# Performance work log

Measured on AMD Instinct MI355X. Metric: run time of the kernel, lower is better.

The kernel has to match this reference:

```python
import jax, jax.numpy as jnp
import numpy as np
import math

HIDDEN = 2048
NUM_HEADS = 16
HEAD_SIZE = HIDDEN // NUM_HEADS
BATCH = 2
SEQ = 2048


def setup_inputs() -> dict:
    key = jax.random.key(0)
    k_x, k_wq, k_bq, k_wo, k_bo = jax.random.split(key, 5)
    scale_in = 1.0 / math.sqrt(HIDDEN)
    return {
        "x": jax.random.normal(k_x, (BATCH, SEQ, HIDDEN), dtype=jnp.float32),
        # torch Linear stored as W[out,in]; we keep the jax-friendly transpose [in,out]
        "Wqkv": jax.random.normal(k_wq, (HIDDEN, 3 * HIDDEN), dtype=jnp.float32) * scale_in,
        "bqkv": jax.random.normal(k_bq, (3 * HIDDEN,), dtype=jnp.float32) * 0.01,
        "Wo": jax.random.normal(k_wo, (HIDDEN, HIDDEN), dtype=jnp.float32) * scale_in,
        "bo": jax.random.normal(k_bo, (HIDDEN,), dtype=jnp.float32) * 0.01,
    }


def reference(x, Wqkv, bqkv, Wo, bo):
    b, s, _ = x.shape
    # fused QKV projection; channel layout is (three, num_heads, head_size)
    kqv = x @ Wqkv + bqkv                      # [b, s, 3*hidden]
    kqv = kqv.reshape(b, s, 3, NUM_HEADS, HEAD_SIZE)
    q = kqv[:, :, 0]                           # [b, s, n, h]
    k = kqv[:, :, 1]
    v = kqv[:, :, 2]
    # scores[b, n, s_key, t_query] = K_s . Q_t, scaled
    scores = jnp.einsum('bsnh,btnh->bnst', k, q) / math.sqrt(HEAD_SIZE)
    # faithful to original: keep upper triangle (key <= query), masked entries are exactly -10000
    ones = jnp.ones_like(scores)
    scores = jnp.triu(scores) + (-10000.0) * jnp.tril(ones, k=-1)
    attn = jax.nn.softmax(scores, axis=2)      # softmax over key dim
    out = jnp.einsum('bnkq,bknh->bqnh', attn, v)  # [b, s, n, h]
    out = out.reshape(b, s, NUM_HEADS * HEAD_SIZE)
    return out @ Wo + bo
```

## Files before the change

### kernel.cpp

```cpp
#include <hip/hip_runtime.h>
#include <hip/hip_bf16.h>

typedef __hip_bfloat16 bf16;
typedef __attribute__((ext_vector_type(8))) short short8;
typedef __attribute__((ext_vector_type(8))) unsigned short ushort8;
typedef __attribute__((ext_vector_type(4))) float floatx4;

#define BATCH 2
#define S_LEN 2048
#define NHEAD 16
#define HD 128
#define HIDDEN 2048
#define QSCALE 0.12754435f

static __device__ __forceinline__ unsigned short f2bf(float f) {
    union { float f; unsigned int u; } c; c.f = f;
    unsigned int u = c.u;
    unsigned int rounded = u + 0x7FFF + ((u >> 16) & 1);
    return (unsigned short)(rounded >> 16);
}

__global__ __launch_bounds__(256) void cast_f32_bf16(const float* __restrict__ src,
                                                     bf16* __restrict__ dst) {
    int i = (blockIdx.x * 256 + threadIdx.x) * 8;
    float4 a = *(const float4*)&src[i];
    float4 b = *(const float4*)&src[i + 4];
    ushort8 o;
    o[0] = f2bf(a.x); o[1] = f2bf(a.y); o[2] = f2bf(a.z); o[3] = f2bf(a.w);
    o[4] = f2bf(b.x); o[5] = f2bf(b.y); o[6] = f2bf(b.z); o[7] = f2bf(b.w);
    *(ushort8*)&dst[i] = o;
}

__global__ __launch_bounds__(256) void cast_transpose(const float* __restrict__ src,
                                                      bf16* __restrict__ dst,
                                                      int R, int C) {
    __shared__ unsigned short t[32][33];
    int tx = threadIdx.x & 31, ty = threadIdx.x >> 5;
    int c0 = blockIdx.x * 32, r0 = blockIdx.y * 32;
#pragma unroll
    for (int i = 0; i < 4; i++) {
        int r = r0 + ty + i * 8;
        t[ty + i * 8][tx] = f2bf(src[(size_t)r * C + c0 + tx]);
    }
    __syncthreads();
#pragma unroll
    for (int i = 0; i < 4; i++) {
        int cc = c0 + ty + i * 8;
        ((unsigned short*)dst)[(size_t)cc * R + r0 + tx] = t[tx][ty + i * 8];
    }
}

__global__ __launch_bounds__(256) void gemm_bt(const bf16* __restrict__ A,
                                               const bf16* __restrict__ Bt,
                                               const float* __restrict__ bias,
                                               float* __restrict__ C,
                                               bf16* __restrict__ Qb,
                                               bf16* __restrict__ Kb,
                                               bf16* __restrict__ Vt,
                                               int M, int N, int K, int mode) {
    __shared__ __align__(16) bf16 As[128 * 32];
    __shared__ __align__(16) bf16 Bs[128 * 32];

    int tid = threadIdx.x;
    int wave = tid >> 6, lane = tid & 63;
    int quad = lane >> 4, lr = lane & 15;
    int wm = wave >> 1, wn = wave & 1;
    int m0 = blockIdx.y * 128, n0 = blockIdx.x * 128;

    const floatx4 fzero = {0.f, 0.f, 0.f, 0.f};
    floatx4 acc[4][4];
#pragma unroll
    for (int i = 0; i < 4; i++)
#pragma unroll
        for (int j = 0; j < 4; j++) acc[i][j] = fzero;

    int rsub = lane >> 2;
    int csub = (lane & 3) * 8;
    const bf16* gA0 = A + (size_t)(m0 + wave * 32 + rsub) * K + csub;
    const bf16* gA1 = gA0 + (size_t)16 * K;
    const bf16* gB0 = Bt + (size_t)(n0 + wave * 32 + rsub) * K + csub;
    const bf16* gB1 = gB0 + (size_t)16 * K;
    bf16* lA0 = As + wave * 1024;
    bf16* lA1 = As + wave * 1024 + 512;
    bf16* lB0 = Bs + wave * 1024;
    bf16* lB1 = Bs + wave * 1024 + 512;

    for (int kt = 0; kt < K; kt += 32) {
        __builtin_amdgcn_global_load_lds(
            (const __attribute__((address_space(1))) void*)(gA0 + kt),
            (__attribute__((address_space(3))) void*)lA0, 16, 0, 0);
        __builtin_amdgcn_global_load_lds(
            (const __attribute__((address_space(1))) void*)(gA1 + kt),
            (__attribute__((address_space(3))) void*)lA1, 16, 0, 0);
        __builtin_amdgcn_global_load_lds(
            (const __attribute__((address_space(1))) void*)(gB0 + kt),
            (__attribute__((address_space(3))) void*)lB0, 16, 0, 0);
        __builtin_amdgcn_global_load_lds(
            (const __attribute__((address_space(1))) void*)(gB1 + kt),
            (__attribute__((address_space(3))) void*)lB1, 16, 0, 0);
        __syncthreads();

        short8 aF[4], bF[4];
#pragma unroll
        for (int i = 0; i < 4; i++)
            aF[i] = *(const short8*)(As + (wm * 64 + i * 16 + lr) * 32 + quad * 8);
#pragma unroll
        for (int j = 0; j < 4; j++)
            bF[j] = *(const short8*)(Bs + (wn * 64 + j * 16 + lr) * 32 + quad * 8);
#pragma unroll
        for (int i = 0; i < 4; i++)
#pragma unroll
            for (int j = 0; j < 4; j++)
                acc[i][j] = __builtin_amdgcn_mfma_f32_16x16x32_bf16(aF[i], bF[j], acc[i][j], 0, 0, 0);
        __syncthreads();
    }

#pragma unroll
    for (int i = 0; i < 4; i++) {
#pragma unroll
        for (int j = 0; j < 4; j++) {
            int gcn = n0 + wn * 64 + j * 16 + lr;
            float bv = bias[gcn];
#pragma unroll
            for (int reg = 0; reg < 4; reg++) {
                int gm = m0 + wm * 64 + i * 16 + quad * 4 + reg;
                float v = acc[i][j][reg] + bv;
                if (mode == 0) {
                    int t = gcn >> 11, hh = (gcn >> 7) & 15, d = gcn & 127;
                    int bb = gm >> 11, s = gm & 2047;
                    size_t hb = (size_t)(bb * NHEAD + hh);
                    if (t == 0) {
                        Qb[(hb * S_LEN + s) * HD + d] = __float2bfloat16(v * QSCALE);
                    } else if (t == 1) {
                        Kb[(hb * S_LEN + s) * HD + d] = __float2bfloat16(v);
                    } else {
                        Vt[(hb * HD + d) * S_LEN + s] = __float2bfloat16(v);
                    }
                } else {
                    C[(size_t)gm * N + gcn] = v;
                }
            }
        }
    }
}

#define PSTR 134
__global__ __launch_bounds__(256, 1) void attn_kernel(const bf16* __restrict__ Qb,
                                                      const bf16* __restrict__ Kb,
                                                      const bf16* __restrict__ Vt,
                                                      bf16* __restrict__ Obuf) {
    __shared__ __align__(16) bf16 Ks[128 * 128];
    __shared__ __align__(16) bf16 Vs[128 * 128];
    __shared__ __align__(16) bf16 Ps[4][32 * PSTR];

    int tid = threadIdx.x;
    int wave = tid >> 6, lane = tid & 63;
    int quad = lane >> 4, lr = lane & 15;
    int srow = lane >> 4;
    int head = blockIdx.x, p = blockIdx.y, b = blockIdx.z;
    size_t hb = (size_t)(b * NHEAD + head);
    const bf16* Qbase = Qb + hb * S_LEN * HD;
    const bf16* Kbase = Kb + hb * S_LEN * HD;
    const bf16* Vbase = Vt + hb * (size_t)HD * S_LEN;

    const floatx4 fzero = {0.f, 0.f, 0.f, 0.f};
    const float MASKV = -30000.f;

    for (int sub = 0; sub < 2; sub++) {
        int qt = sub ? (15 - p) : p;
        int q0 = qt * 128;
        int niter = qt + 1;

        short8 qF[2][4];
#pragma unroll
        for (int mt = 0; mt < 2; mt++)
#pragma unroll
            for (int kc = 0; kc < 4; kc++)
                qF[mt][kc] = *(const short8*)&Qbase[(size_t)(q0 + wave * 32 + mt * 16 + lr) * HD + kc * 32 + quad * 8];

        floatx4 Oacc[2][8];
        float mrow[2][4], lrow[2][4];
#pragma unroll
        for (int mt = 0; mt < 2; mt++) {
#pragma unroll
            for (int dn = 0; dn < 8; dn++) Oacc[mt][dn] = fzero;
#pragma unroll
            for (int r = 0; r < 4; r++) { mrow[mt][r] = -30000.f; lrow[mt][r] = 0.f; }
        }

        for (int kt = 0; kt < niter; kt++) {
            int ks0 = kt * 128;
            __syncthreads();
#pragma unroll
            for (int i = 0; i < 8; i++) {
                int rl = wave * 32 + i * 4 + srow;
                int gc = lr ^ (rl & 15);
                __builtin_amdgcn_global_load_lds(
                    (const __attribute__((address_space(1))) void*)(Kbase + (size_t)(ks0 + rl) * HD + gc * 8),
                    (__attribute__((address_space(3))) void*)(Ks + (wave * 32 + i * 4) * 128), 16, 0, 0);
                __builtin_amdgcn_global_load_lds(
                    (const __attribute__((address_space(1))) void*)(Vbase + (size_t)rl * S_LEN + ks0 + gc * 8),
                    (__attribute__((address_space(3))) void*)(Vs + (wave * 32 + i * 4) * 128), 16, 0, 0);
            }
            __syncthreads();

            floatx4 sc[2][8];
#pragma unroll
            for (int mt = 0; mt < 2; mt++)
#pragma unroll
                for (int nt = 0; nt < 8; nt++) sc[mt][nt] = fzero;
#pragma unroll
            for (int kc = 0; kc < 4; kc++)
#pragma unroll
                for (int nt = 0; nt < 8; nt++) {
                    short8 kf = *(const short8*)&Ks[(nt * 16 + lr) * 128 + (((kc * 4 + quad) ^ lr) & 15) * 8];
#pragma unroll
                    for (int mt = 0; mt < 2; mt++)
                        sc[mt][nt] = __builtin_amdgcn_mfma_f32_16x16x32_bf16(qF[mt][kc], kf, sc[mt][nt], 0, 0, 0);
                }
            if (kt == qt) {
#pragma unroll
                for (int mt = 0; mt < 2; mt++)
#pragma unroll
                    for (int nt = 0; nt < 8; nt++)
#pragma unroll
                        for (int reg = 0; reg < 4; reg++) {
                            int qg = wave * 32 + mt * 16 + quad * 4 + reg;
                            int kg = nt * 16 + lr;
                            if (kg > qg) sc[mt][nt][reg] = MASKV;
                        }
            }
#pragma unroll
            for (int mt = 0; mt < 2; mt++) {
                float pm[4], alpha[4], rs[4];
#pragma unroll
                for (int r = 0; r < 4; r++) {
                    pm[r] = sc[mt][0][r];
#pragma unroll
                    for (int nt = 1; nt < 8; nt++) pm[r] = fmaxf(pm[r], sc[mt][nt][r]);
                }
#pragma unroll
                for (int off = 1; off < 16; off <<= 1)
#pragma unroll
                    for (int r = 0; r < 4; r++) pm[r] = fmaxf(pm[r], __shfl_xor(pm[r], off, 64));
#pragma unroll
                for (int r = 0; r < 4; r++) {
                    float mn = fmaxf(mrow[mt][r], pm[r]);
                    alpha[r] = __builtin_amdgcn_exp2f(mrow[mt][r] - mn);
                    mrow[mt][r] = mn;
                    rs[r] = 0.f;
                }
#pragma unroll
                for (int nt = 0; nt < 8; nt++)
#pragma unroll
                    for (int r = 0; r < 4; r++) {
                        float pv = __builtin_amdgcn_exp2f(sc[mt][nt][r] - mrow[mt][r]);
                        rs[r] += pv;
                        Ps[wave][(mt * 16 + quad * 4 + r) * PSTR + nt * 16 + lr] = __float2bfloat16(pv);
                    }
#pragma unroll
                for (int off = 1; off < 16; off <<= 1)
#pragma unroll
                    for (int r = 0; r < 4; r++) rs[r] += __shfl_xor(rs[r], off, 64);
#pragma unroll
                for (int r = 0; r < 4; r++) lrow[mt][r] = lrow[mt][r] * alpha[r] + rs[r];
#pragma unroll
                for (int dn = 0; dn < 8; dn++)
#pragma unroll
                    for (int r = 0; r < 4; r++) Oacc[mt][dn][r] *= alpha[r];
            }
#pragma unroll
            for (int st = 0; st < 4; st++) {
                short8 aP[2];
#pragma unroll
                for (int mt = 0; mt < 2; mt++)
                    aP[mt] = *(const short8*)&Ps[wave][(mt * 16 + lr) * PSTR + st * 32 + quad * 8];
#pragma unroll
                for (int dn = 0; dn < 8; dn++) {
                    short8 vf = *(const short8*)&Vs[(dn * 16 + lr) * 128 + (((st * 4 + quad) ^ lr) & 15) * 8];
#pragma unroll
                    for (int mt = 0; mt < 2; mt++)
                        Oacc[mt][dn] = __builtin_amdgcn_mfma_f32_16x16x32_bf16(aP[mt], vf, Oacc[mt][dn], 0, 0, 0);
                }
            }
        }

#pragma unroll
        for (int mt = 0; mt < 2; mt++)
#pragma unroll
            for (int reg = 0; reg < 4; reg++) {
                float inv = 1.0f / lrow[mt][reg];
                int qg = q0 + wave * 32 + mt * 16 + quad * 4 + reg;
#pragma unroll
                for (int dn = 0; dn < 8; dn++) {
                    int d = dn * 16 + lr;
                    Obuf[((size_t)(b * S_LEN + qg)) * HIDDEN + head * HD + d] =
                        __float2bfloat16(Oacc[mt][dn][reg] * inv);
                }
            }
    }
}

extern "C" void kernel_launch(void* const* d_in, const int* in_sizes, int n_in,
                              void* d_out, int out_size, void* d_ws, size_t ws_size,
                              hipStream_t stream) {
    (void)in_sizes; (void)n_in; (void)out_size; (void)ws_size;
    const float* x    = (const float*)d_in[0];
    const float* Wqkv = (const float*)d_in[1];
    const float* bqkv = (const float*)d_in[2];
    const float* Wo   = (const float*)d_in[3];
    const float* bo   = (const float*)d_in[4];
    float* out = (float*)d_out;

    bf16* ws = (bf16*)d_ws;
    bf16* Xb    = ws;
    bf16* Obuf  = ws;
    bf16* WqkvT = ws + (size_t)8388608;
    bf16* WoT   = WqkvT;
    bf16* Qb    = WqkvT + (size_t)12582912;
    bf16* Kb    = Qb + (size_t)8388608;
    bf16* Vt    = Kb + (size_t)8388608;

    cast_f32_bf16<<<4096, 256, 0, stream>>>(x, Xb);
    cast_transpose<<<dim3(192, 64), 256, 0, stream>>>(Wqkv, WqkvT, 2048, 6144);
    gemm_bt<<<dim3(48, 32), 256, 0, stream>>>(Xb, WqkvT, bqkv, nullptr,
                                              Qb, Kb, Vt, 4096, 6144, 2048, 0);
    cast_transpose<<<dim3(64, 64), 256, 0, stream>>>(Wo, WoT, 2048, 2048);
    attn_kernel<<<dim3(16, 8, 2), 256, 0, stream>>>(Qb, Kb, Vt, Obuf);
    gemm_bt<<<dim3(16, 32), 256, 0, stream>>>(Obuf, WoT, bo, out,
                                              nullptr, nullptr, nullptr, 4096, 2048, 2048, 1);
}
```

Measured before the change: 460.3 us.

## Halve attention key tile to 64 for two blocks per CU; split GEMM kernels

The attention kernel now processes keys in 64-wide tiles instead of 128. This shrinks K/V/P shared memory and the score registers so two blocks can share a CU (launch_bounds 256,2), at the cost of twice as many loop iterations and more syncs. The V tile swizzle and the diagonal masking are adjusted for the new tile width. The mode-switched GEMM is split into a QKV-scatter kernel and a separate output GEMM, which removes runtime branching from the epilogue.

```diff
diff --git a/kernel.cpp b/kernel.cpp
--- a/kernel.cpp
+++ b/kernel.cpp
@@ -53,11 +53,10 @@
 __global__ __launch_bounds__(256) void gemm_bt(const bf16* __restrict__ A,
                                                const bf16* __restrict__ Bt,
                                                const float* __restrict__ bias,
-                                               float* __restrict__ C,
                                                bf16* __restrict__ Qb,
                                                bf16* __restrict__ Kb,
                                                bf16* __restrict__ Vt,
-                                               int M, int N, int K, int mode) {
+                                               int K) {
     __shared__ __align__(16) bf16 As[128 * 32];
     __shared__ __align__(16) bf16 Bs[128 * 32];
 
@@ -125,32 +124,105 @@
             for (int reg = 0; reg < 4; reg++) {
                 int gm = m0 + wm * 64 + i * 16 + quad * 4 + reg;
                 float v = acc[i][j][reg] + bv;
-                if (mode == 0) {
-                    int t = gcn >> 11, hh = (gcn >> 7) & 15, d = gcn & 127;
-                    int bb = gm >> 11, s = gm & 2047;
-                    size_t hb = (size_t)(bb * NHEAD + hh);
-                    if (t == 0) {
-                        Qb[(hb * S_LEN + s) * HD + d] = __float2bfloat16(v * QSCALE);
-                    } else if (t == 1) {
-                        Kb[(hb * S_LEN + s) * HD + d] = __float2bfloat16(v);
-                    } else {
-                        Vt[(hb * HD + d) * S_LEN + s] = __float2bfloat16(v);
-                    }
+                int t = gcn >> 11, hh = (gcn >> 7) & 15, d = gcn & 127;
+                int bb = gm >> 11, s = gm & 2047;
+                size_t hb = (size_t)(bb * NHEAD + hh);
+                if (t == 0) {
+                    Qb[(hb * S_LEN + s) * HD + d] = __float2bfloat16(v * QSCALE);
+                } else if (t == 1) {
+                    Kb[(hb * S_LEN + s) * HD + d] = __float2bfloat16(v);
                 } else {
-                    C[(size_t)gm * N + gcn] = v;
+                    Vt[(hb * HD + d) * S_LEN + s] = __float2bfloat16(v);
                 }
             }
         }
     }
 }
 
-#define PSTR 134
-__global__ __launch_bounds__(256, 1) void attn_kernel(const bf16* __restrict__ Qb,
+__global__ __launch_bounds__(256) void gemm_out(const bf16* __restrict__ A,
+                                                const bf16* __restrict__ Bt,
+                                                const float* __restrict__ bias,
+                                                float* __restrict__ C,
+                                                int N, int K) {
+    __shared__ __align__(16) bf16 As[128 * 32];
+    __shared__ __align__(16) bf16 Bs[128 * 32];
+
+    int tid = threadIdx.x;
+    int wave = tid >> 6, lane = tid & 63;
+    int quad = lane >> 4, lr = lane & 15;
+    int wm = wave >> 1, wn = wave & 1;
+    int m0 = blockIdx.y * 128, n0 = blockIdx.x * 128;
+
+    const floatx4 fzero = {0.f, 0.f, 0.f, 0.f};
+    floatx4 acc[4][4];
+#pragma unroll
+    for (int i = 0; i < 4; i++)
+#pragma unroll
+        for (int j = 0; j < 4; j++) acc[i][j] = fzero;
+
+    int rsub = lane >> 2;
+    int csub = (lane & 3) * 8;
+    const bf16* gA0 = A + (size_t)(m0 + wave * 32 + rsub) * K + csub;
+    const bf16* gA1 = gA0 + (size_t)16 * K;
+    const bf16* gB0 = Bt + (size_t)(n0 + wave * 32 + rsub) * K + csub;
+    const bf16* gB1 = gB0 + (size_t)16 * K;
+    bf16* lA0 = As + wave * 1024;
+    bf16* lA1 = As + wave * 1024 + 512;
+    bf16* lB0 = Bs + wave * 1024;
+    bf16* lB1 = Bs + wave * 1024 + 512;
+
+    for (int kt = 0; kt < K; kt += 32) {
+        __builtin_amdgcn_global_load_lds(
+            (const __attribute__((address_space(1))) void*)(gA0 + kt),
+            (__attribute__((address_space(3))) void*)lA0, 16, 0, 0);
+        __builtin_amdgcn_global_load_lds(
+            (const __attribute__((address_space(1))) void*)(gA1 + kt),
+            (__attribute__((address_space(3))) void*)lA1, 16, 0, 0);
+        __builtin_amdgcn_global_load_lds(
+            (const __attribute__((address_space(1))) void*)(gB0 + kt),
+            (__attribute__((address_space(3))) void*)lB0, 16, 0, 0);
+        __builtin_amdgcn_global_load_lds(
+            (const __attribute__((address_space(1))) void*)(gB1 + kt),
+            (__attribute__((address_space(3))) void*)lB1, 16, 0, 0);
+        __syncthreads();
+
+        short8 aF[4], bF[4];
+#pragma unroll
+        for (int i = 0; i < 4; i++)
+            aF[i] = *(const short8*)(As + (wm * 64 + i * 16 + lr) * 32 + quad * 8);
+#pragma unroll
+        for (int j = 0; j < 4; j++)
+            bF[j] = *(const short8*)(Bs + (wn * 64 + j * 16 + lr) * 32 + quad * 8);
+#pragma unroll
+        for (int i = 0; i < 4; i++)
+#pragma unroll
+            for (int j = 0; j < 4; j++)
+                acc[i][j] = __builtin_amdgcn_mfma_f32_16x16x32_bf16(aF[i], bF[j], acc[i][j], 0, 0, 0);
+        __syncthreads();
+    }
+
+#pragma unroll
+    for (int i = 0; i < 4; i++) {
+#pragma unroll
+        for (int j = 0; j < 4; j++) {
+            int gcn = n0 + wn * 64 + j * 16 + lr;
+            float bv = bias[gcn];
+#pragma unroll
+            for (int reg = 0; reg < 4; reg++) {
+                int gm = m0 + wm * 64 + i * 16 + quad * 4 + reg;
+                C[(size_t)gm * N + gcn] = acc[i][j][reg] + bv;
+            }
+        }
+    }
+}
+
+#define PSTR 72
+__global__ __launch_bounds__(256, 2) void attn_kernel(const bf16* __restrict__ Qb,
                                                       const bf16* __restrict__ Kb,
                                                       const bf16* __restrict__ Vt,
                                                       bf16* __restrict__ Obuf) {
-    __shared__ __align__(16) bf16 Ks[128 * 128];
-    __shared__ __align__(16) bf16 Vs[128 * 128];
+    __shared__ __align__(16) bf16 Ks[64 * 128];
+    __shared__ __align__(16) bf16 Vs[128 * 64];
     __shared__ __align__(16) bf16 Ps[4][32 * PSTR];
 
     int tid = threadIdx.x;
@@ -169,7 +241,7 @@
     for (int sub = 0; sub < 2; sub++) {
         int qt = sub ? (15 - p) : p;
         int q0 = qt * 128;
-        int niter = qt + 1;
+        int niter = 2 * qt + 2;
 
         short8 qF[2][4];
 #pragma unroll
@@ -189,44 +261,50 @@
         }
 
         for (int kt = 0; kt < niter; kt++) {
-            int ks0 = kt * 128;
+            int ks0 = kt * 64;
             __syncthreads();
 #pragma unroll
-            for (int i = 0; i < 8; i++) {
-                int rl = wave * 32 + i * 4 + srow;
+            for (int i = 0; i < 4; i++) {
+                int rl = wave * 16 + i * 4 + srow;
                 int gc = lr ^ (rl & 15);
                 __builtin_amdgcn_global_load_lds(
                     (const __attribute__((address_space(1))) void*)(Kbase + (size_t)(ks0 + rl) * HD + gc * 8),
-                    (__attribute__((address_space(3))) void*)(Ks + (wave * 32 + i * 4) * 128), 16, 0, 0);
+                    (__attribute__((address_space(3))) void*)(Ks + (wave * 16 + i * 4) * 128), 16, 0, 0);
+            }
+#pragma unroll
+            for (int i = 0; i < 4; i++) {
+                int vr = wave * 32 + i * 8 + (lane >> 3);
+                int gvc = (lane & 7) ^ (vr & 7);
                 __builtin_amdgcn_global_load_lds(
-                    (const __attribute__((address_space(1))) void*)(Vbase + (size_t)rl * S_LEN + ks0 + gc * 8),
-                    (__attribute__((address_space(3))) void*)(Vs + (wave * 32 + i * 4) * 128), 16, 0, 0);
+                    (const __attribute__((address_space(1))) void*)(Vbase + (size_t)vr * S_LEN + ks0 + gvc * 8),
+                    (__attribute__((address_space(3))) void*)(Vs + (wave * 32 + i * 8) * 64), 16, 0, 0);
             }
             __syncthreads();
 
-            floatx4 sc[2][8];
+            floatx4 sc[2][4];
 #pragma unroll
             for (int mt = 0; mt < 2; mt++)
 #pragma unroll
-                for (int nt = 0; nt < 8; nt++) sc[mt][nt] = fzero;
+                for (int nt = 0; nt < 4; nt++) sc[mt][nt] = fzero;
 #pragma unroll
             for (int kc = 0; kc < 4; kc++)
 #pragma unroll
-                for (int nt = 0; nt < 8; nt++) {
+                for (int nt = 0; nt < 4; nt++) {
                     short8 kf = *(const short8*)&Ks[(nt * 16 + lr) * 128 + (((kc * 4 + quad) ^ lr) & 15) * 8];
 #pragma unroll
                     for (int mt = 0; mt < 2; mt++)
                         sc[mt][nt] = __builtin_amdgcn_mfma_f32_16x16x32_bf16(qF[mt][kc], kf, sc[mt][nt], 0, 0, 0);
                 }
-            if (kt == qt) {
+            if (kt >= 2 * qt) {
+                int koff = (kt - 2 * qt) * 64;
 #pragma unroll
                 for (int mt = 0; mt < 2; mt++)
 #pragma unroll
-                    for (int nt = 0; nt < 8; nt++)
+                    for (int nt = 0; nt < 4; nt++)
 #pragma unroll
                         for (int reg = 0; reg < 4; reg++) {
                             int qg = wave * 32 + mt * 16 + quad * 4 + reg;
-                            int kg = nt * 16 + lr;
+                            int kg = koff + nt * 16 + lr;
                             if (kg > qg) sc[mt][nt][reg] = MASKV;
                         }
             }
@@ -237,7 +315,7 @@
                 for (int r = 0; r < 4; r++) {
                     pm[r] = sc[mt][0][r];
 #pragma unroll
-                    for (int nt = 1; nt < 8; nt++) pm[r] = fmaxf(pm[r], sc[mt][nt][r]);
+                    for (int nt = 1; nt < 4; nt++) pm[r] = fmaxf(pm[r], sc[mt][nt][r]);
                 }
 #pragma unroll
                 for (int off = 1; off < 16; off <<= 1)
@@ -251,7 +329,7 @@
                     rs[r] = 0.f;
                 }
 #pragma unroll
-                for (int nt = 0; nt < 8; nt++)
+                for (int nt = 0; nt < 4; nt++)
 #pragma unroll
                     for (int r = 0; r < 4; r++) {
                         float pv = __builtin_amdgcn_exp2f(sc[mt][nt][r] - mrow[mt][r]);
@@ -270,14 +348,14 @@
                     for (int r = 0; r < 4; r++) Oacc[mt][dn][r] *= alpha[r];
             }
 #pragma unroll
-            for (int st = 0; st < 4; st++) {
+            for (int st = 0; st < 2; st++) {
                 short8 aP[2];
 #pragma unroll
                 for (int mt = 0; mt < 2; mt++)
                     aP[mt] = *(const short8*)&Ps[wave][(mt * 16 + lr) * PSTR + st * 32 + quad * 8];
 #pragma unroll
                 for (int dn = 0; dn < 8; dn++) {
-                    short8 vf = *(const short8*)&Vs[(dn * 16 + lr) * 128 + (((st * 4 + quad) ^ lr) & 15) * 8];
+                    short8 vf = *(const short8*)&Vs[(dn * 16 + lr) * 64 + (((st * 4 + quad) ^ (lr & 7)) & 7) * 8];
 #pragma unroll
                     for (int mt = 0; mt < 2; mt++)
                         Oacc[mt][dn] = __builtin_amdgcn_mfma_f32_16x16x32_bf16(aP[mt], vf, Oacc[mt][dn], 0, 0, 0);
@@ -323,10 +401,8 @@
 
     cast_f32_bf16<<<4096, 256, 0, stream>>>(x, Xb);
     cast_transpose<<<dim3(192, 64), 256, 0, stream>>>(Wqkv, WqkvT, 2048, 6144);
-    gemm_bt<<<dim3(48, 32), 256, 0, stream>>>(Xb, WqkvT, bqkv, nullptr,
-                                              Qb, Kb, Vt, 4096, 6144, 2048, 0);
+    gemm_bt<<<dim3(48, 32), 256, 0, stream>>>(Xb, WqkvT, bqkv, Qb, Kb, Vt, 2048);
     cast_transpose<<<dim3(64, 64), 256, 0, stream>>>(Wo, WoT, 2048, 2048);
     attn_kernel<<<dim3(16, 8, 2), 256, 0, stream>>>(Qb, Kb, Vt, Obuf);
-    gemm_bt<<<dim3(16, 32), 256, 0, stream>>>(Obuf, WoT, bo, out,
-                                              nullptr, nullptr, nullptr, 4096, 2048, 2048, 1);
-}
+    gemm_out<<<dim3(16, 32), 256, 0, stream>>>(Obuf, WoT, bo, out, 2048, 2048);
+}
```

Result: faster. 445.6 us (-3.2%).
